# Kernel optimization log

Hardware: AMD Instinct MI355X
Metric: run time of the kernel (lower is better)

The kernel has to match this reference:

```python
import jax, jax.numpy as jnp
import numpy as np

D = 2048   # num_vars
H = 4096   # hidden width (2*D, pyro default)
B = 8192   # batch


def _made_masks():
    #   input degrees  : 1..D
    #   hidden degrees : arange(H) % (D-1) + 1  (in 1..D-1)
    #   output degrees : 1..D, strict inequality for the output layer
    inp_deg = np.arange(1, D + 1)
    hid_deg = np.arange(H) % (D - 1) + 1
    out_deg = np.arange(1, D + 1)
    m1 = (hid_deg[:, None] >= inp_deg[None, :]).astype(np.float32)  # [H, D]
    m2 = (hid_deg[:, None] >= hid_deg[None, :]).astype(np.float32)  # [H, H]
    m3 = (out_deg[:, None] > hid_deg[None, :]).astype(np.float32)   # [D, H]
    return jnp.asarray(m1), jnp.asarray(m2), jnp.asarray(m3)

M1, M2, M3 = _made_masks()
PERM = jnp.arange(D)  # permutation=torch.arange(num_vars) -> identity gather


def setup_inputs() -> dict:
    key = jax.random.key(0)
    ks = jax.random.split(key, 7)
    value = jax.random.randint(ks[0], (B, D), 0, 2).astype(jnp.float32)
    s1 = 1.0 / np.sqrt(D)
    s2 = 1.0 / np.sqrt(H)
    W1 = jax.random.uniform(ks[1], (H, D), minval=-s1, maxval=s1, dtype=jnp.float32)
    b1 = jax.random.uniform(ks[2], (H,), minval=-s1, maxval=s1, dtype=jnp.float32)
    W2 = jax.random.uniform(ks[3], (H, H), minval=-s2, maxval=s2, dtype=jnp.float32)
    b2 = jax.random.uniform(ks[4], (H,), minval=-s2, maxval=s2, dtype=jnp.float32)
    W3 = jax.random.uniform(ks[5], (D, H), minval=-s2, maxval=s2, dtype=jnp.float32)
    b3 = jax.random.uniform(ks[6], (D,), minval=-s2, maxval=s2, dtype=jnp.float32)
    return {"value": value, "W1": W1, "b1": b1, "W2": W2, "b2": b2,
            "W3": W3, "b3": b3}


def reference(value, W1, b1, W2, b2, W3, b3):
    h1 = jax.nn.relu(value @ (W1 * M1).T + b1)          # [B, H]
    h2 = jax.nn.relu(h1 @ (W2 * M2).T + b2)             # [B, H]
    logits = h2 @ (W3 * M3).T + b3                      # [B, D]
    logits = logits[:, PERM]                            # identity permutation gather
    # Bernoulli(logits).log_prob(value) = value*logits - softplus(logits)
    log_prob = (value * logits - jax.nn.softplus(logits)).sum(axis=1)  # [B]
    return log_prob
```

## Files before the change

kernel.cpp:

```cpp
#include <hip/hip_runtime.h>
#include <hip/hip_bf16.h>
#include <cstdint>

typedef short short8 __attribute__((ext_vector_type(8)));
typedef float floatx4 __attribute__((ext_vector_type(4)));
typedef float f32x4 __attribute__((ext_vector_type(4)));
typedef unsigned short u16;
typedef unsigned short u16x4 __attribute__((ext_vector_type(4)));

#define BB 8192
#define DD 2048
#define HH 4096

static __device__ __forceinline__ u16 f2bf(float x) {
  __hip_bfloat16 h = __float2bfloat16(x);
  return __builtin_bit_cast(u16, h);
}

static __device__ __forceinline__ float bf2f(u16 x) {
  unsigned int u = ((unsigned int)x) << 16;
  return __builtin_bit_cast(float, u);
}

static __device__ __forceinline__ void glds16(const u16* g, u16* l) {
  __builtin_amdgcn_global_load_lds(
      (const __attribute__((address_space(1))) void*)g,
      (__attribute__((address_space(3))) void*)l, 16, 0, 0);
}

__global__ void cvt_value_kernel(const float* __restrict__ in, u16* __restrict__ out, int n4) {
  int idx = blockIdx.x * blockDim.x + threadIdx.x;
  int stride = gridDim.x * blockDim.x;
  for (int i = idx; i < n4; i += stride) {
    f32x4 v = reinterpret_cast<const f32x4*>(in)[i];
    u16x4 o = { f2bf(v[0]), f2bf(v[1]), f2bf(v[2]), f2bf(v[3]) };
    reinterpret_cast<u16x4*>(out)[i] = o;
  }
}

template<int MODE>
__global__ __launch_bounds__(256) void mask_cvt_tile(const float* __restrict__ in,
                                                     u16* __restrict__ out, int W) {
  const int r0 = blockIdx.y * 64;
  const int c0 = blockIdx.x * 64;
  const int re = r0 + 63, ce = c0 + 63;

  bool zero;
  if (MODE == 0) {
    int rmaxd = (r0 >= 2047) ? ((re <= 4093) ? (re - 2047) : 2046)
                             : ((re <= 2046) ? re : 2046);
    zero = (c0 > rmaxd);
  } else if (MODE == 1) {
    int rmaxd = (r0 >= 2047) ? ((re <= 4093) ? (re - 2047) : 2046)
                             : ((re <= 2046) ? re : 2046);
    int cmind = (c0 >= 2047) ? ((ce >= 4094) ? 0 : (c0 - 2047))
                             : ((ce >= 2047) ? 0 : c0);
    zero = (cmind > rmaxd);
  } else {
    int cmind = (c0 >= 2047) ? ((ce >= 4094) ? 0 : (c0 - 2047))
                             : ((ce >= 2047) ? 0 : c0);
    zero = (re <= cmind);
  }

  const int tr = threadIdx.x >> 4;
  const int tc = (threadIdx.x & 15) * 4;

  if (zero) {
    u16x4 z = {0, 0, 0, 0};
#pragma unroll
    for (int rr = 0; rr < 64; rr += 16)
      *(u16x4*)&out[(size_t)(r0 + tr + rr) * W + c0 + tc] = z;
    return;
  }

#pragma unroll
  for (int rr = 0; rr < 64; rr += 16) {
    int r = r0 + tr + rr;
    int rdeg = r % 2047;
    f32x4 v = *(const f32x4*)&in[(size_t)r * W + c0 + tc];
    u16x4 o;
#pragma unroll
    for (int e = 0; e < 4; ++e) {
      int c = c0 + tc + e;
      bool keep;
      if (MODE == 0)      keep = (c <= rdeg);
      else if (MODE == 1) keep = ((c % 2047) <= rdeg);
      else                keep = (r > (c % 2047));
      o[e] = keep ? f2bf(v[e]) : (u16)0;
    }
    *(u16x4*)&out[(size_t)r * W + c0 + tc] = o;
  }
}

template<int MASKM>
__global__ __launch_bounds__(512, 2) void gemm256_kernel(
    const u16* __restrict__ A, const u16* __restrict__ Bw,
    const float* __restrict__ bias, u16* __restrict__ C,
    int M, int N, int K)
{
  __shared__ u16 ls[2][32768];

  const int tid  = threadIdx.x;
  const int wid  = tid >> 6;
  const int lane = tid & 63;
  const int wm = wid >> 2, wn = wid & 3;
  const int l15 = lane & 15, lhi = lane >> 4;

  const int wg = blockIdx.x;
  const int xcd = wg & 7, j = wg >> 3;
  const int yb = (xcd << 2) | (j & 3);
  const int p  = j >> 2;
  const int brow = yb * 256;
  int cols[2];
  cols[0] = (p < 4) ? p : p + 4;
  cols[1] = (p < 4) ? 7 - p : 19 - p;

  const int arow_ = tid >> 3;
  const int agsub = (tid & 7) ^ (arow_ & 7);
  size_t aB[4];
  aB[0] = (size_t)(brow +   0 + arow_) * K + agsub * 8;
  aB[1] = (size_t)(brow + 128 + arow_) * K + agsub * 8;
  aB[2] = (size_t)(brow +  64 + arow_) * K + agsub * 8;
  aB[3] = (size_t)(brow + 192 + arow_) * K + agsub * 8;
  const int aCh[4] = {0, 1024, 512, 1536};

#pragma unroll 1
  for (int t = 0; t < 2; ++t) {
    const int bcol = cols[t] * 256;

    int rmax;
    {
      int sC = bcol, e = bcol + 255;
      if (e <= 2046)       rmax = e;
      else if (sC <= 2046) rmax = 2046;
      else { int em = e - 2047; rmax = (em <= 2046) ? em : 2046; }
    }
    int r1end = ((rmax >> 6) + 1) << 6; if (r1end > K) r1end = K;
    int run2start, r2end;
    if (MASKM == 1) { run2start = r1end; r2end = r1end; }
    else {
      run2start = (1984 > r1end) ? 1984 : r1end;
      r2end = (((2047 + rmax) >> 6) + 1) << 6; if (r2end > K) r2end = K;
      if (r2end < run2start) r2end = run2start;
    }
    const int n1 = r1end >> 6;
    const int nt = n1 + ((r2end - run2start) >> 6);
    const int roff = run2start - r1end;
    const int nte = nt + ((MASKM != 1 && r2end < K) ? 1 : 0);

    size_t bB[2][2];
#pragma unroll
    for (int u = 0; u < 2; ++u)
#pragma unroll
      for (int c = 0; c < 2; ++c)
        bB[u][c] = (size_t)(bcol + u * 128 + arow_ + 64 * c) * K + agsub * 8;

    floatx4 acc[8][4];
#pragma unroll
    for (int i = 0; i < 8; ++i)
#pragma unroll
      for (int jj = 0; jj < 4; ++jj)
        acc[i][jj] = (floatx4){0.f, 0.f, 0.f, 0.f};

#define K0F(jx) (((jx) >= nt) ? (K - 64) : (((jx) << 6) + (((jx) >= n1) ? roff : 0)))
#define ST_A(slot_, idx_, k0v) glds16(A + aB[idx_] + (k0v), (u16*)&ls[slot_][(aCh[idx_] + tid) * 8])
#define ST_B(slot_, u_, k0v) do { \
      glds16(Bw + bB[u_][0] + (k0v), (u16*)&ls[slot_][(2048 + (u_) * 1024 + tid) * 8]); \
      glds16(Bw + bB[u_][1] + (k0v), (u16*)&ls[slot_][(2048 + (u_) * 1024 + tid + 512) * 8]); \
    } while (0)
#define ST_TILE(slot_, k0v) do { \
      ST_A(slot_, 0, k0v); ST_A(slot_, 1, k0v); ST_A(slot_, 2, k0v); ST_A(slot_, 3, k0v); \
      ST_B(slot_, 0, k0v); ST_B(slot_, 1, k0v); \
    } while (0)

    {
      const int k00 = K0F(0);
      ST_TILE(0, k00);
    }
    asm volatile("s_waitcnt vmcnt(0)" ::: "memory");
    __builtin_amdgcn_sched_barrier(0);
    __builtin_amdgcn_s_barrier();
    __builtin_amdgcn_sched_barrier(0);

#pragma unroll 1
    for (int i = 0; i < nte; ++i) {
      const int s = i & 1, o = s ^ 1;
      const u16* sA = &ls[s][0];
      const u16* sB = &ls[s][16384];
      const bool g1 = (i + 1 < nte);
      short8 af0[4], af1[4], af2[4], af3[4], bf0[4], bf1[4];

      if (g1) {
        const int k1 = K0F(i + 1);
        ST_TILE(o, k1);
      }

#define RD_A_TO(dst_, q_, ks_) do { \
        _Pragma("unroll") \
        for (int mi = 0; mi < 4; ++mi) { \
          int row = wm * 128 + (q_) * 64 + mi * 16 + l15; \
          int ch = row * 8 + (((ks_) * 4 + lhi) ^ (row & 7)); \
          dst_[mi] = *(const short8*)&sA[ch * 8]; \
        } } while (0)
#define RD_B_TO(dst_, ks_) do { \
        _Pragma("unroll") \
        for (int ni = 0; ni < 4; ++ni) { \
          int row = wn * 64 + ni * 16 + l15; \
          int ch = row * 8 + (((ks_) * 4 + lhi) ^ (row & 7)); \
          dst_[ni] = *(const short8*)&sB[ch * 8]; \
        } } while (0)
#define MFMA16(q_, afv_, bfv_) do { \
        _Pragma("unroll") \
        for (int mi = 0; mi < 4; ++mi) \
          _Pragma("unroll") \
          for (int ni = 0; ni < 4; ++ni) \
            acc[(q_) * 4 + mi][ni] = __builtin_amdgcn_mfma_f32_16x16x32_bf16( \
                afv_[mi], bfv_[ni], acc[(q_) * 4 + mi][ni], 0, 0, 0); \
        } while (0)

      RD_A_TO(af0, 0, 0); RD_B_TO(bf0, 0);
      __builtin_amdgcn_sched_barrier(0);
      RD_A_TO(af1, 0, 1); RD_B_TO(bf1, 1);
      __builtin_amdgcn_sched_barrier(0);

      asm volatile("s_waitcnt lgkmcnt(8)" ::: "memory");
      __builtin_amdgcn_sched_barrier(0);
      __builtin_amdgcn_s_setprio(1);
      MFMA16(0, af0, bf0);
      __builtin_amdgcn_s_setprio(0);
      RD_A_TO(af2, 1, 0);
      __builtin_amdgcn_sched_barrier(0);
      RD_A_TO(af3, 1, 1);
      __builtin_amdgcn_sched_barrier(0);

      asm volatile("s_waitcnt lgkmcnt(8)" ::: "memory");
      __builtin_amdgcn_sched_barrier(0);
      __builtin_amdgcn_s_setprio(1);
      MFMA16(0, af1, bf1);
      __builtin_amdgcn_s_setprio(0);
      __builtin_amdgcn_sched_barrier(0);

      asm volatile("s_waitcnt lgkmcnt(4)" ::: "memory");
      __builtin_amdgcn_sched_barrier(0);
      __builtin_amdgcn_s_setprio(1);
      MFMA16(1, af2, bf0);
      __builtin_amdgcn_s_setprio(0);
      __builtin_amdgcn_sched_barrier(0);

      asm volatile("s_waitcnt lgkmcnt(0)" ::: "memory");
      __builtin_amdgcn_sched_barrier(0);
      __builtin_amdgcn_s_setprio(1);
      MFMA16(1, af3, bf1);
      __builtin_amdgcn_s_setprio(0);

      asm volatile("s_waitcnt vmcnt(0)" ::: "memory");
      __builtin_amdgcn_sched_barrier(0);
      __builtin_amdgcn_s_barrier();
      __builtin_amdgcn_sched_barrier(0);
#undef RD_A_TO
#undef RD_B_TO
#undef MFMA16
    }

#pragma unroll
    for (int mi = 0; mi < 8; ++mi) {
      int row = brow + wm * 128 + (mi >> 2) * 64 + (mi & 3) * 16 + lhi * 4;
#pragma unroll
      for (int ni = 0; ni < 4; ++ni) {
        int col = bcol + wn * 64 + ni * 16 + l15;
        float bv = bias[col];
#pragma unroll
        for (int e = 0; e < 4; ++e) {
          float v = acc[mi][ni][e] + bv;
          v = fmaxf(v, 0.0f);
          C[(size_t)(row + e) * N + col] = f2bf(v);
        }
      }
    }
    __syncthreads();
#undef K0F
#undef ST_A
#undef ST_B
#undef ST_TILE
  }
}

__global__ __launch_bounds__(512, 1) void gemm3p_kernel(
    const u16* __restrict__ A,
    const u16* __restrict__ Bw,
    const float* __restrict__ bias,
    const u16* __restrict__ vbf,
    float* __restrict__ outp,
    int M, int N, int K)
{
  __shared__ u16 ls[2][24576];

  const int tid  = threadIdx.x;
  const int wid  = tid >> 6;
  const int lane = tid & 63;
  const int wm = wid >> 2, wn = wid & 3;
  const int l15 = lane & 15, lhi = lane >> 4;

  const int wg = blockIdx.x;
  const int xcd = wg & 7, j = wg >> 3;
  const int yb = (xcd << 3) | (j & 7);
  const int q  = j >> 3;
  const int brow = yb * 128;
  int sgs[2] = { q, 7 - q };

  size_t aOff[2];
#pragma unroll
  for (int u = 0; u < 2; ++u) {
    int ch = tid + 512 * u;
    int row = ch >> 3, sub = ch & 7;
    aOff[u] = (size_t)(brow + row) * K + (sub ^ (row & 7)) * 8;
  }
  int bRow[4], bSsub[4];
#pragma unroll
  for (int u = 0; u < 4; ++u) {
    int ch = tid + 512 * u;
    bRow[u] = ch >> 3;
    bSsub[u] = (ch & 7) ^ (bRow[u] & 7);
  }

#pragma unroll 1
  for (int t = 0; t < 2; ++t) {
    const int bcol = sgs[t] * 256;
    const int rmax = bcol + 254;

    int r1end = ((rmax >> 6) + 1) << 6; if (r1end > K) r1end = K;
    int run2start = (1984 > r1end) ? 1984 : r1end;
    int r2end = (((2047 + rmax) >> 6) + 1) << 6; if (r2end > K) r2end = K;
    if (r2end < run2start) r2end = run2start;
    const int n1 = r1end >> 6;
    const int nt = n1 + ((r2end - run2start) >> 6);
    const int roff = run2start - r1end;
    const int nte = nt + ((r2end < K) ? 1 : 0);

    size_t bOff[4];
#pragma unroll
    for (int u = 0; u < 4; ++u)
      bOff[u] = (size_t)(bcol + bRow[u]) * K + bSsub[u] * 8;

    floatx4 acc[4][4];
#pragma unroll
    for (int i = 0; i < 4; ++i)
#pragma unroll
      for (int jj = 0; jj < 4; ++jj)
        acc[i][jj] = (floatx4){0.f, 0.f, 0.f, 0.f};

#define K0G(jx) (((jx) >= nt) ? (K - 64) : (((jx) << 6) + (((jx) >= n1) ? roff : 0)))
#define ST3(slot_, k0v) do { \
      glds16(A  + aOff[0] + (k0v), (u16*)&ls[slot_][tid * 8]); \
      glds16(A  + aOff[1] + (k0v), (u16*)&ls[slot_][(512 + tid) * 8]); \
      glds16(Bw + bOff[0] + (k0v), (u16*)&ls[slot_][(1024 + tid) * 8]); \
      glds16(Bw + bOff[1] + (k0v), (u16*)&ls[slot_][(1536 + tid) * 8]); \
      glds16(Bw + bOff[2] + (k0v), (u16*)&ls[slot_][(2048 + tid) * 8]); \
      glds16(Bw + bOff[3] + (k0v), (u16*)&ls[slot_][(2560 + tid) * 8]); \
    } while (0)

    ST3(0, K0G(0));
    asm volatile("s_waitcnt vmcnt(0)" ::: "memory");
    __builtin_amdgcn_sched_barrier(0);
    __builtin_amdgcn_s_barrier();
    __builtin_amdgcn_sched_barrier(0);

#pragma unroll 1
    for (int i = 0; i < nte; ++i) {
      const int s = i & 1, o = s ^ 1;
      const u16* sA = &ls[s][0];
      const u16* sB = &ls[s][8192];
      const bool g1 = (i + 1 < nte);
      short8 af0[4], af1[4], bf0[4], bf1[4];

      if (g1) ST3(o, K0G(i + 1));

#pragma unroll
      for (int mi = 0; mi < 4; ++mi) {
        int row = wm * 64 + mi * 16 + l15;
        af0[mi] = *(const short8*)&sA[(row * 8 + (lhi ^ (row & 7))) * 8];
      }
#pragma unroll
      for (int ni = 0; ni < 4; ++ni) {
        int row = wn * 64 + ni * 16 + l15;
        bf0[ni] = *(const short8*)&sB[(row * 8 + (lhi ^ (row & 7))) * 8];
      }
      __builtin_amdgcn_sched_barrier(0);
#pragma unroll
      for (int mi = 0; mi < 4; ++mi) {
        int row = wm * 64 + mi * 16 + l15;
        af1[mi] = *(const short8*)&sA[(row * 8 + ((4 + lhi) ^ (row & 7))) * 8];
      }
#pragma unroll
      for (int ni = 0; ni < 4; ++ni) {
        int row = wn * 64 + ni * 16 + l15;
        bf1[ni] = *(const short8*)&sB[(row * 8 + ((4 + lhi) ^ (row & 7))) * 8];
      }
      __builtin_amdgcn_sched_barrier(0);

      asm volatile("s_waitcnt lgkmcnt(8)" ::: "memory");
      __builtin_amdgcn_sched_barrier(0);
      __builtin_amdgcn_s_setprio(1);
#pragma unroll
      for (int mi = 0; mi < 4; ++mi)
#pragma unroll
        for (int ni = 0; ni < 4; ++ni)
          acc[mi][ni] = __builtin_amdgcn_mfma_f32_16x16x32_bf16(af0[mi], bf0[ni], acc[mi][ni], 0, 0, 0);
      __builtin_amdgcn_s_setprio(0);
      __builtin_amdgcn_sched_barrier(0);

      asm volatile("s_waitcnt lgkmcnt(0)" ::: "memory");
      __builtin_amdgcn_sched_barrier(0);
      __builtin_amdgcn_s_setprio(1);
#pragma unroll
      for (int mi = 0; mi < 4; ++mi)
#pragma unroll
        for (int ni = 0; ni < 4; ++ni)
          acc[mi][ni] = __builtin_amdgcn_mfma_f32_16x16x32_bf16(af1[mi], bf1[ni], acc[mi][ni], 0, 0, 0);
      __builtin_amdgcn_s_setprio(0);

      asm volatile("s_waitcnt vmcnt(0)" ::: "memory");
      __builtin_amdgcn_sched_barrier(0);
      __builtin_amdgcn_s_barrier();
      __builtin_amdgcn_sched_barrier(0);
    }
#undef K0G
#undef ST3

#pragma unroll
    for (int mi = 0; mi < 4; ++mi) {
#pragma unroll
      for (int e = 0; e < 4; ++e) {
        int row = brow + wm * 64 + mi * 16 + lhi * 4 + e;
        float partial = 0.0f;
#pragma unroll
        for (int ni = 0; ni < 4; ++ni) {
          int col = bcol + wn * 64 + ni * 16 + l15;
          float l = acc[mi][ni][e] + bias[col];
          float v = bf2f(vbf[(size_t)row * N + col]);
          float sp = fmaxf(l, 0.0f) + __logf(1.0f + __expf(-fabsf(l)));
          partial += v * l - sp;
        }
#pragma unroll
        for (int off = 1; off < 16; off <<= 1)
          partial += __shfl_xor(partial, off, 64);
        if (l15 == 0) atomicAdd(&outp[row], partial);
      }
    }
  }
}

extern "C" void kernel_launch(void* const* d_in, const int* in_sizes, int n_in,
                              void* d_out, int out_size, void* d_ws, size_t ws_size,
                              hipStream_t stream) {
  const float* value = (const float*)d_in[0];
  const float* W1 = (const float*)d_in[1];
  const float* b1 = (const float*)d_in[2];
  const float* W2 = (const float*)d_in[3];
  const float* b2 = (const float*)d_in[4];
  const float* W3 = (const float*)d_in[5];
  const float* b3 = (const float*)d_in[6];
  float* out = (float*)d_out;

  char* ws = (char*)d_ws;
  u16* vbf = (u16*)(ws);
  u16* w1m = (u16*)(ws + 33554432ULL);
  u16* w2m = (u16*)(ws + 50331648ULL);
  u16* w3m = (u16*)(ws + 83886080ULL);
  u16* h1  = (u16*)(ws + 100663296ULL);
  u16* h2  = (u16*)(ws + 167772160ULL);

  hipMemsetAsync(d_out, 0, (size_t)out_size * sizeof(float), stream);

  cvt_value_kernel<<<2048, 256, 0, stream>>>(value, vbf, (BB * DD) / 4);
  mask_cvt_tile<0><<<dim3(DD / 64, HH / 64), 256, 0, stream>>>(W1, w1m, DD);
  mask_cvt_tile<1><<<dim3(HH / 64, HH / 64), 256, 0, stream>>>(W2, w2m, HH);
  mask_cvt_tile<2><<<dim3(HH / 64, DD / 64), 256, 0, stream>>>(W3, w3m, HH);

  gemm256_kernel<1><<<256, 512, 0, stream>>>(vbf, w1m, b1, h1, BB, HH, DD);
  gemm256_kernel<2><<<256, 512, 0, stream>>>(h1, w2m, b2, h2, BB, HH, HH);
  gemm3p_kernel<<<256, 512, 0, stream>>>(h2, w3m, b3, vbf, out, BB, DD, HH);
}
```

Before: 372.3 us.

## Split gemm3 column pairs into separate blocks and drop manual MFMA scheduling barriers

```diff
diff --git a/kernel.cpp b/kernel.cpp
--- a/kernel.cpp
+++ b/kernel.cpp
@@ -163,24 +163,20 @@
         acc[i][jj] = (floatx4){0.f, 0.f, 0.f, 0.f};
 
 #define K0F(jx) (((jx) >= nt) ? (K - 64) : (((jx) << 6) + (((jx) >= n1) ? roff : 0)))
-#define ST_A(slot_, idx_, k0v) glds16(A + aB[idx_] + (k0v), (u16*)&ls[slot_][(aCh[idx_] + tid) * 8])
-#define ST_B(slot_, u_, k0v) do { \
-      glds16(Bw + bB[u_][0] + (k0v), (u16*)&ls[slot_][(2048 + (u_) * 1024 + tid) * 8]); \
-      glds16(Bw + bB[u_][1] + (k0v), (u16*)&ls[slot_][(2048 + (u_) * 1024 + tid + 512) * 8]); \
-    } while (0)
 #define ST_TILE(slot_, k0v) do { \
-      ST_A(slot_, 0, k0v); ST_A(slot_, 1, k0v); ST_A(slot_, 2, k0v); ST_A(slot_, 3, k0v); \
-      ST_B(slot_, 0, k0v); ST_B(slot_, 1, k0v); \
-    } while (0)
-
-    {
-      const int k00 = K0F(0);
-      ST_TILE(0, k00);
-    }
+    glds16(A + aB[0] + (k0v), (u16*)&ls[slot_][(aCh[0] + tid) * 8]); \
+    glds16(A + aB[1] + (k0v), (u16*)&ls[slot_][(aCh[1] + tid) * 8]); \
+    glds16(A + aB[2] + (k0v), (u16*)&ls[slot_][(aCh[2] + tid) * 8]); \
+    glds16(A + aB[3] + (k0v), (u16*)&ls[slot_][(aCh[3] + tid) * 8]); \
+    glds16(Bw + bB[0][0] + (k0v), (u16*)&ls[slot_][(2048 + tid) * 8]); \
+    glds16(Bw + bB[0][1] + (k0v), (u16*)&ls[slot_][(2048 + tid + 512) * 8]); \
+    glds16(Bw + bB[1][0] + (k0v), (u16*)&ls[slot_][(3072 + tid) * 8]); \
+    glds16(Bw + bB[1][1] + (k0v), (u16*)&ls[slot_][(3072 + tid + 512) * 8]); \
+  } while (0)
+
+    ST_TILE(0, K0F(0));
     asm volatile("s_waitcnt vmcnt(0)" ::: "memory");
-    __builtin_amdgcn_sched_barrier(0);
     __builtin_amdgcn_s_barrier();
-    __builtin_amdgcn_sched_barrier(0);
 
 #pragma unroll 1
     for (int i = 0; i < nte; ++i) {
@@ -188,75 +184,46 @@
       const u16* sA = &ls[s][0];
       const u16* sB = &ls[s][16384];
       const bool g1 = (i + 1 < nte);
-      short8 af0[4], af1[4], af2[4], af3[4], bf0[4], bf1[4];
-
-      if (g1) {
-        const int k1 = K0F(i + 1);
-        ST_TILE(o, k1);
-      }
+
+      if (g1) ST_TILE(o, K0F(i + 1));
 
 #define RD_A_TO(dst_, q_, ks_) do { \
+      _Pragma("unroll") \
+      for (int mi = 0; mi < 4; ++mi) { \
+        int row = wm * 128 + (q_) * 64 + mi * 16 + l15; \
+        int ch = row * 8 + (((ks_) * 4 + lhi) ^ (row & 7)); \
+        dst_[mi] = *(const short8*)&sA[ch * 8]; \
+      } } while (0)
+#define RD_B_TO(dst_, ks_) do { \
+      _Pragma("unroll") \
+      for (int ni = 0; ni < 4; ++ni) { \
+        int row = wn * 64 + ni * 16 + l15; \
+        int ch = row * 8 + (((ks_) * 4 + lhi) ^ (row & 7)); \
+        dst_[ni] = *(const short8*)&sB[ch * 8]; \
+      } } while (0)
+#define MFMA16(q_, afv_, bfv_) do { \
+      _Pragma("unroll") \
+      for (int mi = 0; mi < 4; ++mi) \
         _Pragma("unroll") \
-        for (int mi = 0; mi < 4; ++mi) { \
-          int row = wm * 128 + (q_) * 64 + mi * 16 + l15; \
-          int ch = row * 8 + (((ks_) * 4 + lhi) ^ (row & 7)); \
-          dst_[mi] = *(const short8*)&sA[ch * 8]; \
-        } } while (0)
-#define RD_B_TO(dst_, ks_) do { \
-        _Pragma("unroll") \
-        for (int ni = 0; ni < 4; ++ni) { \
-          int row = wn * 64 + ni * 16 + l15; \
-          int ch = row * 8 + (((ks_) * 4 + lhi) ^ (row & 7)); \
-          dst_[ni] = *(const short8*)&sB[ch * 8]; \
-        } } while (0)
-#define MFMA16(q_, afv_, bfv_) do { \
-        _Pragma("unroll") \
-        for (int mi = 0; mi < 4; ++mi) \
-          _Pragma("unroll") \
-          for (int ni = 0; ni < 4; ++ni) \
-            acc[(q_) * 4 + mi][ni] = __builtin_amdgcn_mfma_f32_16x16x32_bf16( \
-                afv_[mi], bfv_[ni], acc[(q_) * 4 + mi][ni], 0, 0, 0); \
-        } while (0)
-
-      RD_A_TO(af0, 0, 0); RD_B_TO(bf0, 0);
-      __builtin_amdgcn_sched_barrier(0);
-      RD_A_TO(af1, 0, 1); RD_B_TO(bf1, 1);
-      __builtin_amdgcn_sched_barrier(0);
-
-      asm volatile("s_waitcnt lgkmcnt(8)" ::: "memory");
-      __builtin_amdgcn_sched_barrier(0);
-      __builtin_amdgcn_s_setprio(1);
-      MFMA16(0, af0, bf0);
-      __builtin_amdgcn_s_setprio(0);
-      RD_A_TO(af2, 1, 0);
-      __builtin_amdgcn_sched_barrier(0);
-      RD_A_TO(af3, 1, 1);
-      __builtin_amdgcn_sched_barrier(0);
-
-      asm volatile("s_waitcnt lgkmcnt(8)" ::: "memory");
-      __builtin_amdgcn_sched_barrier(0);
-      __builtin_amdgcn_s_setprio(1);
-      MFMA16(0, af1, bf1);
-      __builtin_amdgcn_s_setprio(0);
-      __builtin_amdgcn_sched_barrier(0);
-
-      asm volatile("s_waitcnt lgkmcnt(4)" ::: "memory");
-      __builtin_amdgcn_sched_barrier(0);
-      __builtin_amdgcn_s_setprio(1);
-      MFMA16(1, af2, bf0);
-      __builtin_amdgcn_s_setprio(0);
-      __builtin_amdgcn_sched_barrier(0);
-
-      asm volatile("s_waitcnt lgkmcnt(0)" ::: "memory");
-      __builtin_amdgcn_sched_barrier(0);
-      __builtin_amdgcn_s_setprio(1);
-      MFMA16(1, af3, bf1);
-      __builtin_amdgcn_s_setprio(0);
+        for (int ni = 0; ni < 4; ++ni) \
+          acc[(q_) * 4 + mi][ni] = __builtin_amdgcn_mfma_f32_16x16x32_bf16( \
+              afv_[mi], bfv_[ni], acc[(q_) * 4 + mi][ni], 0, 0, 0); \
+      } while (0)
+
+      {
+        short8 af0[4], af1[4], af2[4], af3[4], bf0[4], bf1[4];
+        RD_A_TO(af0, 0, 0); RD_B_TO(bf0, 0);
+        MFMA16(0, af0, bf0);
+        RD_A_TO(af1, 0, 1); RD_B_TO(bf1, 1);
+        MFMA16(0, af1, bf1);
+        RD_A_TO(af2, 1, 0);
+        MFMA16(1, af2, bf0);
+        RD_A_TO(af3, 1, 1);
+        MFMA16(1, af3, bf1);
+      }
 
       asm volatile("s_waitcnt vmcnt(0)" ::: "memory");
-      __builtin_amdgcn_sched_barrier(0);
       __builtin_amdgcn_s_barrier();
-      __builtin_amdgcn_sched_barrier(0);
 #undef RD_A_TO
 #undef RD_B_TO
 #undef MFMA16
@@ -279,13 +246,11 @@
     }
     __syncthreads();
 #undef K0F
-#undef ST_A
-#undef ST_B
 #undef ST_TILE
   }
 }
 
-__global__ __launch_bounds__(512, 1) void gemm3p_kernel(
+__global__ __launch_bounds__(512, 2) void gemm3p_kernel(
     const u16* __restrict__ A,
     const u16* __restrict__ Bw,
     const float* __restrict__ bias,
@@ -304,9 +269,9 @@
   const int wg = blockIdx.x;
   const int xcd = wg & 7, j = wg >> 3;
   const int yb = (xcd << 3) | (j & 7);
-  const int q  = j >> 3;
+  const int sg = 7 - (j >> 3);
   const int brow = yb * 128;
-  int sgs[2] = { q, 7 - q };
+  const int bcol = sg * 256;
 
   size_t aOff[2];
 #pragma unroll
@@ -323,58 +288,54 @@
     bSsub[u] = (ch & 7) ^ (bRow[u] & 7);
   }
 
-#pragma unroll 1
-  for (int t = 0; t < 2; ++t) {
-    const int bcol = sgs[t] * 256;
-    const int rmax = bcol + 254;
-
-    int r1end = ((rmax >> 6) + 1) << 6; if (r1end > K) r1end = K;
-    int run2start = (1984 > r1end) ? 1984 : r1end;
-    int r2end = (((2047 + rmax) >> 6) + 1) << 6; if (r2end > K) r2end = K;
-    if (r2end < run2start) r2end = run2start;
-    const int n1 = r1end >> 6;
-    const int nt = n1 + ((r2end - run2start) >> 6);
-    const int roff = run2start - r1end;
-    const int nte = nt + ((r2end < K) ? 1 : 0);
-
-    size_t bOff[4];
-#pragma unroll
-    for (int u = 0; u < 4; ++u)
-      bOff[u] = (size_t)(bcol + bRow[u]) * K + bSsub[u] * 8;
-
-    floatx4 acc[4][4];
-#pragma unroll
-    for (int i = 0; i < 4; ++i)
-#pragma unroll
-      for (int jj = 0; jj < 4; ++jj)
-        acc[i][jj] = (floatx4){0.f, 0.f, 0.f, 0.f};
+  const int rmax = bcol + 254;
+
+  int r1end = ((rmax >> 6) + 1) << 6; if (r1end > K) r1end = K;
+  int run2start = (1984 > r1end) ? 1984 : r1end;
+  int r2end = (((2047 + rmax) >> 6) + 1) << 6; if (r2end > K) r2end = K;
+  if (r2end < run2start) r2end = run2start;
+  const int n1 = r1end >> 6;
+  const int nt = n1 + ((r2end - run2start) >> 6);
+  const int roff = run2start - r1end;
+  const int nte = nt + ((r2end < K) ? 1 : 0);
+
+  size_t bOff[4];
+#pragma unroll
+  for (int u = 0; u < 4; ++u)
+    bOff[u] = (size_t)(bcol + bRow[u]) * K + bSsub[u] * 8;
+
+  floatx4 acc[4][4];
+#pragma unroll
+  for (int i = 0; i < 4; ++i)
+#pragma unroll
+    for (int jj = 0; jj < 4; ++jj)
+      acc[i][jj] = (floatx4){0.f, 0.f, 0.f, 0.f};
 
 #define K0G(jx) (((jx) >= nt) ? (K - 64) : (((jx) << 6) + (((jx) >= n1) ? roff : 0)))
 #define ST3(slot_, k0v) do { \
-      glds16(A  + aOff[0] + (k0v), (u16*)&ls[slot_][tid * 8]); \
-      glds16(A  + aOff[1] + (k0v), (u16*)&ls[slot_][(512 + tid) * 8]); \
-      glds16(Bw + bOff[0] + (k0v), (u16*)&ls[slot_][(1024 + tid) * 8]); \
-      glds16(Bw + bOff[1] + (k0v), (u16*)&ls[slot_][(1536 + tid) * 8]); \
-      glds16(Bw + bOff[2] + (k0v), (u16*)&ls[slot_][(2048 + tid) * 8]); \
-      glds16(Bw + bOff[3] + (k0v), (u16*)&ls[slot_][(2560 + tid) * 8]); \
-    } while (0)
-
-    ST3(0, K0G(0));
-    asm volatile("s_waitcnt vmcnt(0)" ::: "memory");
-    __builtin_amdgcn_sched_barrier(0);
-    __builtin_amdgcn_s_barrier();
-    __builtin_amdgcn_sched_barrier(0);
+    glds16(A  + aOff[0] + (k0v), (u16*)&ls[slot_][tid * 8]); \
+    glds16(A  + aOff[1] + (k0v), (u16*)&ls[slot_][(512 + tid) * 8]); \
+    glds16(Bw + bOff[0] + (k0v), (u16*)&ls[slot_][(1024 + tid) * 8]); \
+    glds16(Bw + bOff[1] + (k0v), (u16*)&ls[slot_][(1536 + tid) * 8]); \
+    glds16(Bw + bOff[2] + (k0v), (u16*)&ls[slot_][(2048 + tid) * 8]); \
+    glds16(Bw + bOff[3] + (k0v), (u16*)&ls[slot_][(2560 + tid) * 8]); \
+  } while (0)
+
+  ST3(0, K0G(0));
+  asm volatile("s_waitcnt vmcnt(0)" ::: "memory");
+  __builtin_amdgcn_s_barrier();
 
 #pragma unroll 1
-    for (int i = 0; i < nte; ++i) {
-      const int s = i & 1, o = s ^ 1;
-      const u16* sA = &ls[s][0];
-      const u16* sB = &ls[s][8192];
-      const bool g1 = (i + 1 < nte);
+  for (int i = 0; i < nte; ++i) {
+    const int s = i & 1, o = s ^ 1;
+    const u16* sA = &ls[s][0];
+    const u16* sB = &ls[s][8192];
+    const bool g1 = (i + 1 < nte);
+
+    if (g1) ST3(o, K0G(i + 1));
+
+    {
       short8 af0[4], af1[4], bf0[4], bf1[4];
-
-      if (g1) ST3(o, K0G(i + 1));
-
 #pragma unroll
       for (int mi = 0; mi < 4; ++mi) {
         int row = wm * 64 + mi * 16 + l15;
@@ -385,7 +346,11 @@
         int row = wn * 64 + ni * 16 + l15;
         bf0[ni] = *(const short8*)&sB[(row * 8 + (lhi ^ (row & 7))) * 8];
       }
-      __builtin_amdgcn_sched_barrier(0);
+#pragma unroll
+      for (int mi = 0; mi < 4; ++mi)
+#pragma unroll
+        for (int ni = 0; ni < 4; ++ni)
+          acc[mi][ni] = __builtin_amdgcn_mfma_f32_16x16x32_bf16(af0[mi], bf0[ni], acc[mi][ni], 0, 0, 0);
 #pragma unroll
       for (int mi = 0; mi < 4; ++mi) {
         int row = wm * 64 + mi * 16 + l15;
@@ -396,56 +361,37 @@
         int row = wn * 64 + ni * 16 + l15;
         bf1[ni] = *(const short8*)&sB[(row * 8 + ((4 + lhi) ^ (row & 7))) * 8];
       }
-      __builtin_amdgcn_sched_barrier(0);
-
-      asm volatile("s_waitcnt lgkmcnt(8)" ::: "memory");
-      __builtin_amdgcn_sched_barrier(0);
-      __builtin_amdgcn_s_setprio(1);
-#pragma unroll
-      for (int mi = 0; mi < 4; ++mi)
-#pragma unroll
-        for (int ni = 0; ni < 4; ++ni)
-          acc[mi][ni] = __builtin_amdgcn_mfma_f32_16x16x32_bf16(af0[mi], bf0[ni], acc[mi][ni], 0, 0, 0);
-      __builtin_amdgcn_s_setprio(0);
-      __builtin_amdgcn_sched_barrier(0);
-
-      asm volatile("s_waitcnt lgkmcnt(0)" ::: "memory");
-      __builtin_amdgcn_sched_barrier(0);
-      __builtin_amdgcn_s_setprio(1);
 #pragma unroll
       for (int mi = 0; mi < 4; ++mi)
 #pragma unroll
         for (int ni = 0; ni < 4; ++ni)
           acc[mi][ni] = __builtin_amdgcn_mfma_f32_16x16x32_bf16(af1[mi], bf1[ni], acc[mi][ni], 0, 0, 0);
-      __builtin_amdgcn_s_setprio(0);
-
-      asm volatile("s_waitcnt vmcnt(0)" ::: "memory");
-      __builtin_amdgcn_sched_barrier(0);
-      __builtin_amdgcn_s_barrier();
-      __builtin_amdgcn_sched_barrier(0);
-    }
+    }
+
+    asm volatile("s_waitcnt vmcnt(0)" ::: "memory");
+    __builtin_amdgcn_s_barrier();
+  }
 #undef K0G
 #undef ST3
 
 #pragma unroll
-    for (int mi = 0; mi < 4; ++mi) {
-#pragma unroll
-      for (int e = 0; e < 4; ++e) {
-        int row = brow + wm * 64 + mi * 16 + lhi * 4 + e;
-        float partial = 0.0f;
-#pragma unroll
-        for (int ni = 0; ni < 4; ++ni) {
-          int col = bcol + wn * 64 + ni * 16 + l15;
-          float l = acc[mi][ni][e] + bias[col];
-          float v = bf2f(vbf[(size_t)row * N + col]);
-          float sp = fmaxf(l, 0.0f) + __logf(1.0f + __expf(-fabsf(l)));
-          partial += v * l - sp;
-        }
-#pragma unroll
-        for (int off = 1; off < 16; off <<= 1)
-          partial += __shfl_xor(partial, off, 64);
-        if (l15 == 0) atomicAdd(&outp[row], partial);
-      }
+  for (int mi = 0; mi < 4; ++mi) {
+#pragma unroll
+    for (int e = 0; e < 4; ++e) {
+      int row = brow + wm * 64 + mi * 16 + lhi * 4 + e;
+      float partial = 0.0f;
+#pragma unroll
+      for (int ni = 0; ni < 4; ++ni) {
+        int col = bcol + wn * 64 + ni * 16 + l15;
+        float l = acc[mi][ni][e] + bias[col];
+        float v = bf2f(vbf[(size_t)row * N + col]);
+        float sp = fmaxf(l, 0.0f) + __logf(1.0f + __expf(-fabsf(l)));
+        partial += v * l - sp;
+      }
+#pragma unroll
+      for (int off = 1; off < 16; off <<= 1)
+        partial += __shfl_xor(partial, off, 64);
+      if (l15 == 0) atomicAdd(&outp[row], partial);
     }
   }
 }
@@ -479,5 +425,5 @@
 
   gemm256_kernel<1><<<256, 512, 0, stream>>>(vbf, w1m, b1, h1, BB, HH, DD);
   gemm256_kernel<2><<<256, 512, 0, stream>>>(h1, w2m, b2, h2, BB, HH, HH);
-  gemm3p_kernel<<<256, 512, 0, stream>>>(h2, w3m, b3, vbf, out, BB, DD, HH);
-}
+  gemm3p_kernel<<<512, 512, 0, stream>>>(h2, w3m, b3, vbf, out, BB, DD, HH);
+}
```

Result: faster. 353.9 us (median of 2 runs) (-4.9%).
